# Kernel tuning notes

Hardware: AMD Instinct MI355X
Metric: run time of the kernel (lower is better)

## Reference

```python
import jax, jax.numpy as jnp
import numpy as np

N_NODES = 50000
N_EDGES = 1600000
IN_FEAT = 256
HID = IN_FEAT // 2  # 128
OUT_FEAT = 256


def setup_inputs() -> dict:
    key = jax.random.key(0)
    ks = jax.random.split(key, 10)
    x = jax.random.normal(ks[0], (N_NODES, IN_FEAT), dtype=jnp.float32)
    w = jax.random.uniform(ks[1], (N_EDGES, 1), dtype=jnp.float32)
    src = jax.random.randint(ks[2], (N_EDGES,), 0, N_NODES, dtype=jnp.int32)
    dst = jax.random.randint(ks[3], (N_EDGES,), 0, N_NODES, dtype=jnp.int32)
    s = 1.0 / np.sqrt(IN_FEAT)
    W_node = jax.random.uniform(ks[4], (IN_FEAT, HID), jnp.float32, -s, s)
    b_node = jax.random.uniform(ks[5], (HID,), jnp.float32, -s, s)
    W_edge = jax.random.uniform(ks[6], (IN_FEAT, HID), jnp.float32, -s, s)
    b_edge = jax.random.uniform(ks[7], (HID,), jnp.float32, -s, s)
    s2 = 1.0 / np.sqrt(HID)
    W_mlp = jax.random.uniform(ks[8], (HID, OUT_FEAT), jnp.float32, -s2, s2)
    b_mlp = jax.random.uniform(ks[9], (OUT_FEAT,), jnp.float32, -s2, s2)
    return {"x": x, "w": w, "src": src, "dst": dst,
            "W_node": W_node, "b_node": b_node,
            "W_edge": W_edge, "b_edge": b_edge,
            "W_mlp": W_mlp, "b_mlp": b_mlp}


def reference(x, w, src, dst, W_node, b_node, W_edge, b_edge, W_mlp, b_mlp):
    # message[v] = sum_{(u->v) in E} x[u] * w_e   (src_mul_edge + sum)
    message = jax.ops.segment_sum(x[src] * w, dst, num_segments=x.shape[0])  # [N, in_feat]
    h = (x @ W_node + b_node) + (message @ W_edge + b_edge)  # [N, in_feat//2]
    # NOTE: original uses nn.LeakyReLU(True) -> negative_slope=1.0 (identity);
    # replicated faithfully.
    h = jax.nn.leaky_relu(h, negative_slope=1.0)
    return h @ W_mlp + b_mlp  # [N, out_feat]
```

## Files before the change

kernel.cpp:

```cpp
#include <hip/hip_runtime.h>


constexpr int N_NODES  = 50000;
constexpr int N_EDGES  = 1600000;
constexpr int IN_FEAT  = 256;
constexpr int HID      = 128;
constexpr int OUT_FEAT = 256;

constexpr int BIN_SZ   = 32;
constexpr int N_BINS   = (N_NODES + BIN_SZ - 1) / BIN_SZ;
constexpr int CAPBIN   = 1536;
constexpr int EPB      = 4096;
constexpr int N_CBLK   = (N_EDGES + EPB - 1) / EPB;
constexpr int GRID_M   = (N_NODES + 127) / 128;
constexpr int N_G1BLK  = GRID_M * 2;

typedef __attribute__((ext_vector_type(8))) short bf16x8;
typedef __attribute__((ext_vector_type(8))) unsigned short u16x8;
typedef __attribute__((ext_vector_type(4))) float f32x4;

static __device__ __forceinline__ unsigned short f2bf(float f) {
    unsigned u = __builtin_bit_cast(unsigned, f);
    u += 0x7FFF + ((u >> 16) & 1);
    return (unsigned short)(u >> 16);
}
static __device__ __forceinline__ float bflo(unsigned u) {
    return __builtin_bit_cast(float, u << 16);
}
static __device__ __forceinline__ float bfhi(unsigned u) {
    return __builtin_bit_cast(float, u & 0xFFFF0000u);
}

__global__ __launch_bounds__(256) void k0_convert(
    const float* __restrict__ Wn, const float* __restrict__ We,
    const float* __restrict__ Wm,
    unsigned short* __restrict__ Wcat_t, unsigned short* __restrict__ Wmt)
{
    int n = blockIdx.x;
    int k = threadIdx.x;
    float v = (n < HID) ? Wn[(size_t)k * HID + n] : We[(size_t)k * HID + (n - HID)];
    Wcat_t[(size_t)n * IN_FEAT + k] = f2bf(v);
    if (k < HID) Wmt[(size_t)n * HID + k] = f2bf(Wm[(size_t)k * OUT_FEAT + n]);
}

union SharedU {
    struct {
        int  hist[N_BINS];
        int  gbase[N_BINS];
        int  wsum[8];
        int  stot;
        int2 sorted[EPB];
    } bc;
    struct {
        unsigned short As[128][64];
        unsigned short Bs[128][64];
    } g1;
};

__global__ __launch_bounds__(512, 4) void fuse1(
    const int* __restrict__ src, const int* __restrict__ dst,
    const float* __restrict__ w, int* __restrict__ cursor,
    int2* __restrict__ entries,
    const float* __restrict__ x, const unsigned short* __restrict__ Wcat_t,
    const float* __restrict__ bn, const float* __restrict__ be,
    float* __restrict__ h0, unsigned short* __restrict__ ybf)
{
    __shared__ SharedU sh;
    const int t = threadIdx.x;
    const int wave = t >> 6, lane = t & 63;

    if (blockIdx.x < N_CBLK) {
        const int e0 = blockIdx.x * EPB;

        for (int i = t; i < N_BINS; i += 512) sh.bc.hist[i] = 0;
        __syncthreads();

        int meta[8], wb[8], rk[8], bin[8];
        #pragma unroll
        for (int k = 0; k < 8; ++k) {
            int e = e0 + t + k * 512;
            bin[k] = -1;
            if (e < N_EDGES) {
                int d = dst[e];
                int b = d >> 5;
                bin[k]  = b;
                meta[k] = src[e] | ((d & 31) << 16) | (b << 21);
                wb[k]   = __float_as_int(w[e]);
                rk[k]   = atomicAdd(&sh.bc.hist[b], 1);
            }
        }
        __syncthreads();

        const int b4 = t * 4;
        int c0 = 0, c1 = 0, c2 = 0, c3 = 0;
        if (b4 + 0 < N_BINS) c0 = sh.bc.hist[b4 + 0];
        if (b4 + 1 < N_BINS) c1 = sh.bc.hist[b4 + 1];
        if (b4 + 2 < N_BINS) c2 = sh.bc.hist[b4 + 2];
        if (b4 + 3 < N_BINS) c3 = sh.bc.hist[b4 + 3];
        const int s = c0 + c1 + c2 + c3;
        int pre = s;
        #pragma unroll
        for (int off = 1; off < 64; off <<= 1) {
            int o = __shfl_up(pre, off, 64);
            if (lane >= off) pre += o;
        }
        if (lane == 63) sh.bc.wsum[wave] = pre;
        __syncthreads();
        if (t == 0) {
            int r = 0;
            #pragma unroll
            for (int q = 0; q < 8; ++q) { int v = sh.bc.wsum[q]; sh.bc.wsum[q] = r; r += v; }
            sh.bc.stot = r;
        }
        __syncthreads();
        const int tb = sh.bc.wsum[wave] + pre - s;

        if (b4 + 0 < N_BINS) {
            sh.bc.hist[b4 + 0]  = tb;
            sh.bc.gbase[b4 + 0] = c0 ? atomicAdd(&cursor[b4 + 0], c0) : 0;
        }
        if (b4 + 1 < N_BINS) {
            sh.bc.hist[b4 + 1]  = tb + c0;
            sh.bc.gbase[b4 + 1] = c1 ? atomicAdd(&cursor[b4 + 1], c1) : 0;
        }
        if (b4 + 2 < N_BINS) {
            sh.bc.hist[b4 + 2]  = tb + c0 + c1;
            sh.bc.gbase[b4 + 2] = c2 ? atomicAdd(&cursor[b4 + 2], c2) : 0;
        }
        if (b4 + 3 < N_BINS) {
            sh.bc.hist[b4 + 3]  = tb + c0 + c1 + c2;
            sh.bc.gbase[b4 + 3] = c3 ? atomicAdd(&cursor[b4 + 3], c3) : 0;
        }
        __syncthreads();

        #pragma unroll
        for (int k = 0; k < 8; ++k)
            if (bin[k] >= 0)
                sh.bc.sorted[sh.bc.hist[bin[k]] + rk[k]] = make_int2(meta[k], wb[k]);
        __syncthreads();

        const int tot = sh.bc.stot;
        #pragma unroll
        for (int k = 0; k < 8; ++k) {
            int i = t + k * 512;
            if (i < tot) {
                int2 q = sh.bc.sorted[i];
                int b = ((unsigned)q.x) >> 21;
                int r = i - sh.bc.hist[b];
                int g = sh.bc.gbase[b] + r;
                if (g < CAPBIN)
                    entries[(size_t)b * CAPBIN + g] = make_int2(q.x & 0x1FFFFF, q.y);
            }
        }
    } else {
        const int bid2 = blockIdx.x - N_CBLK;
        const int m0 = (bid2 >> 1) * 128;
        const int nhalf = bid2 & 1;
        const int n0r = nhalf * 128;

        const int wm = wave >> 2, wn = wave & 3;
        const int la = lane & 15, kq = lane >> 4;
        const int srow = t >> 3, sc8 = t & 7;

        f32x4 acc[4][2];
        const f32x4 zero = {0.f, 0.f, 0.f, 0.f};
        #pragma unroll
        for (int i = 0; i < 4; ++i)
            #pragma unroll
            for (int j = 0; j < 2; ++j) acc[i][j] = zero;

        const float4* xg = (const float4*)x;

        for (int kt = 0; kt < 4; ++kt) {
            if (kt) __syncthreads();
            #pragma unroll
            for (int i = 0; i < 2; ++i) {
                int row = srow + i * 64;
                int node = m0 + row;
                float4 v0 = make_float4(0.f, 0.f, 0.f, 0.f), v1 = v0;
                if (node < N_NODES) {
                    v0 = xg[(size_t)node * 64 + kt * 16 + sc8 * 2];
                    v1 = xg[(size_t)node * 64 + kt * 16 + sc8 * 2 + 1];
                }
                u16x8 b;
                b[0] = f2bf(v0.x); b[1] = f2bf(v0.y); b[2] = f2bf(v0.z); b[3] = f2bf(v0.w);
                b[4] = f2bf(v1.x); b[5] = f2bf(v1.y); b[6] = f2bf(v1.z); b[7] = f2bf(v1.w);
                *(u16x8*)&sh.g1.As[row][(sc8 ^ (row & 7)) * 8] = b;
            }
            #pragma unroll
            for (int i = 0; i < 2; ++i) {
                int row = srow + i * 64;
                float4 v = *(const float4*)(
                    Wcat_t + (size_t)(n0r + row) * IN_FEAT + kt * 64 + sc8 * 8);
                *(float4*)&sh.g1.Bs[row][(sc8 ^ (row & 7)) * 8] = v;
            }
            __syncthreads();

            #pragma unroll
            for (int ks = 0; ks < 2; ++ks) {
                bf16x8 a[4], b[2];
                #pragma unroll
                for (int i = 0; i < 4; ++i) {
                    int row = wm * 64 + i * 16 + la;
                    a[i] = *(const bf16x8*)&sh.g1.As[row][((ks * 4 + kq) ^ (row & 7)) * 8];
                }
                #pragma unroll
                for (int j = 0; j < 2; ++j) {
                    int row = wn * 32 + j * 16 + la;
                    b[j] = *(const bf16x8*)&sh.g1.Bs[row][((ks * 4 + kq) ^ (row & 7)) * 8];
                }
                #pragma unroll
                for (int i = 0; i < 4; ++i)
                    #pragma unroll
                    for (int j = 0; j < 2; ++j)
                        acc[i][j] = __builtin_amdgcn_mfma_f32_16x16x32_bf16(
                            a[i], b[j], acc[i][j], 0, 0, 0);
            }
        }

        float bias[2];
        if (nhalf == 0) {
            #pragma unroll
            for (int j = 0; j < 2; ++j) {
                int n = wn * 32 + j * 16 + la;
                bias[j] = bn[n] + be[n];
            }
        }
        #pragma unroll
        for (int i = 0; i < 4; ++i) {
            int mbase = m0 + wm * 64 + i * 16 + kq * 4;
            #pragma unroll
            for (int j = 0; j < 2; ++j) {
                int n = wn * 32 + j * 16 + la;
                #pragma unroll
                for (int r = 0; r < 4; ++r) {
                    int m = mbase + r;
                    if (m < N_NODES) {
                        if (nhalf == 0)
                            h0[(size_t)m * HID + n] = acc[i][j][r] + bias[j];
                        else
                            ybf[(size_t)m * HID + n] = f2bf(acc[i][j][r]);
                    }
                }
            }
        }
    }
}

__global__ __launch_bounds__(512, 4) void fuse2(
    const unsigned short* __restrict__ ybf, const float* __restrict__ h0,
    const int* __restrict__ cursor, const int2* __restrict__ entries,
    const unsigned short* __restrict__ Wmt, const float* __restrict__ bm,
    float* __restrict__ out)
{
    __shared__ unsigned short As[128][128];
    __shared__ int2 sorted[CAPBIN];
    __shared__ int  cnt32[BIN_SZ];
    __shared__ int  offs32[BIN_SZ];

    const int t = threadIdx.x;
    const int wave = t >> 6, lane = t & 63;
    const int m0 = blockIdx.x * 128;
    const int bin0 = blockIdx.x * 4;

    for (int sb = 0; sb < 4; ++sb) {
        const int bin = bin0 + sb;
        const int tot = (bin < N_BINS) ? min(cursor[bin], CAPBIN) : 0;
        if (t < BIN_SZ) cnt32[t] = 0;
        __syncthreads();

        int2 held[3];
        int  hrank[3], hdloc[3];
        #pragma unroll
        for (int k = 0; k < 3; ++k) {
            hdloc[k] = -1;
            int g = t + k * 512;
            if (g < tot) {
                int2 ep = entries[(size_t)bin * CAPBIN + g];
                int dloc = ep.x >> 16;
                held[k]  = make_int2(ep.x & 0xFFFF, ep.y);
                hdloc[k] = dloc;
                hrank[k] = atomicAdd(&cnt32[dloc], 1);
            }
        }
        __syncthreads();

        if (wave == 0) {
            int v = (lane < BIN_SZ) ? cnt32[lane] : 0;
            int sum = v;
            #pragma unroll
            for (int off = 1; off < BIN_SZ; off <<= 1) {
                int o = __shfl_up(sum, off, 64);
                if (lane >= off) sum += o;
            }
            if (lane < BIN_SZ) offs32[lane] = sum - v;
        }
        __syncthreads();

        #pragma unroll
        for (int k = 0; k < 3; ++k)
            if (hdloc[k] >= 0)
                sorted[offs32[hdloc[k]] + hrank[k]] = held[k];
        __syncthreads();

        #pragma unroll
        for (int n4 = 0; n4 < 4; ++n4) {
            const int nl = wave * 4 + n4;
            const int row = sb * 32 + nl;
            const int node = bin * BIN_SZ + nl;
            const int beg = offs32[nl];
            const int c = cnt32[nl];
            float a0 = 0.f, a1 = 0.f;
            int j = 0;
            for (; j + 8 <= c; j += 8) {
                int2 q[8]; unsigned u[8];
                #pragma unroll
                for (int e = 0; e < 8; ++e) q[e] = sorted[beg + j + e];
                #pragma unroll
                for (int e = 0; e < 8; ++e)
                    u[e] = *(const unsigned*)&ybf[(size_t)q[e].x * HID + 2 * lane];
                #pragma unroll
                for (int e = 0; e < 8; ++e) {
                    float wq = __int_as_float(q[e].y);
                    a0 += wq * bflo(u[e]); a1 += wq * bfhi(u[e]);
                }
            }
            for (; j < c; ++j) {
                int2 q = sorted[beg + j];
                unsigned u = *(const unsigned*)&ybf[(size_t)q.x * HID + 2 * lane];
                float wq = __int_as_float(q.y);
                a0 += wq * bflo(u); a1 += wq * bfhi(u);
            }
            float2 hv = make_float2(0.f, 0.f);
            if (node < N_NODES)
                hv = *(const float2*)&h0[(size_t)node * HID + 2 * lane];
            unsigned rp = ((unsigned)f2bf(hv.y + a1) << 16)
                        | (unsigned)f2bf(hv.x + a0);
            int g8 = (lane >> 2) ^ (row & 7);
            *(unsigned*)((char*)&As[row][0] + g8 * 16 + (lane & 3) * 4) = rp;
        }
        __syncthreads();
    }

    const int wm = wave >> 2, wn = wave & 3;
    const int la = lane & 15, kq = lane >> 4;

    f32x4 acc[4][4];
    const f32x4 zero = {0.f, 0.f, 0.f, 0.f};
    #pragma unroll
    for (int i = 0; i < 4; ++i)
        #pragma unroll
        for (int j = 0; j < 4; ++j) acc[i][j] = zero;

    #pragma unroll
    for (int ks = 0; ks < 4; ++ks) {
        bf16x8 a[4], b[4];
        #pragma unroll
        for (int i = 0; i < 4; ++i) {
            int row = wm * 64 + i * 16 + la;
            a[i] = *(const bf16x8*)&As[row][((ks * 4 + kq) ^ (row & 7)) * 8];
        }
        #pragma unroll
        for (int j = 0; j < 4; ++j) {
            int n = wn * 64 + j * 16 + la;
            b[j] = *(const bf16x8*)(Wmt + (size_t)n * HID + ks * 32 + kq * 8);
        }
        #pragma unroll
        for (int i = 0; i < 4; ++i)
            #pragma unroll
            for (int j = 0; j < 4; ++j)
                acc[i][j] = __builtin_amdgcn_mfma_f32_16x16x32_bf16(
                    a[i], b[j], acc[i][j], 0, 0, 0);
    }

    #pragma unroll
    for (int i = 0; i < 4; ++i) {
        int mbase = m0 + wm * 64 + i * 16 + kq * 4;
        #pragma unroll
        for (int j = 0; j < 4; ++j) {
            int n = wn * 64 + j * 16 + la;
            float bv = bm[n];
            #pragma unroll
            for (int r = 0; r < 4; ++r) {
                int m = mbase + r;
                if (m < N_NODES)
                    out[(size_t)m * OUT_FEAT + n] = acc[i][j][r] + bv;
            }
        }
    }
}

extern "C" void kernel_launch(void* const* d_in, const int* in_sizes, int n_in,
                              void* d_out, int out_size, void* d_ws, size_t ws_size,
                              hipStream_t stream) {
    const float* x   = (const float*)d_in[0];
    const float* w   = (const float*)d_in[1];
    const int*   src = (const int*)d_in[2];
    const int*   dst = (const int*)d_in[3];
    const float* Wn  = (const float*)d_in[4];
    const float* bn  = (const float*)d_in[5];
    const float* We  = (const float*)d_in[6];
    const float* be  = (const float*)d_in[7];
    const float* Wm  = (const float*)d_in[8];
    const float* bm  = (const float*)d_in[9];
    float* out = (float*)d_out;

    char* p = (char*)d_ws;
    float*          h0      = (float*)p;          p += (size_t)N_NODES * HID * 4;
    unsigned short* ybf     = (unsigned short*)p; p += (size_t)N_NODES * HID * 2;
    int2*           entries = (int2*)p;           p += (size_t)N_BINS * CAPBIN * 8;
    unsigned short* Wcat_t  = (unsigned short*)p; p += (size_t)256 * IN_FEAT * 2;
    unsigned short* Wmt     = (unsigned short*)p; p += (size_t)OUT_FEAT * HID * 2;
    int*            cursor  = (int*)p;            p += (size_t)N_BINS * 4;

    dim3 blk(256);

    hipMemsetAsync(cursor, 0, (size_t)N_BINS * 4, stream);
    k0_convert<<<256, blk, 0, stream>>>(Wn, We, Wm, Wcat_t, Wmt);
    fuse1<<<N_CBLK + N_G1BLK, dim3(512), 0, stream>>>(
        src, dst, w, cursor, entries, x, Wcat_t, bn, be, h0, ybf);
    fuse2<<<GRID_M, dim3(512), 0, stream>>>(ybf, h0, cursor, entries, Wmt, bm, out);
}
```

Baseline: 270.9 us.

## Launch one fuse2 block per 32-node bin instead of per 128 nodes

fuse2 now handles a single 32-node bin per block rather than looping over four bins serially, and the final MLP GEMM is cut to 32 rows per block. The grid grows from about 391 to about 1563 blocks, and shared memory per block shrinks. The goal is more parallelism and occupancy for the latency-bound gather and sort phase. In exchange, each block reloads the Wmt tile for only 32 rows, and the wm split now gives two waves duplicate-free 16-row slices of a small MFMA.

New measurement: 267.4 us. About the same (-1.3%).

```diff
diff --git a/kernel.cpp b/kernel.cpp
--- a/kernel.cpp
+++ b/kernel.cpp
@@ -253,139 +253,121 @@
     const unsigned short* __restrict__ Wmt, const float* __restrict__ bm,
     float* __restrict__ out)
 {
-    __shared__ unsigned short As[128][128];
     __shared__ int2 sorted[CAPBIN];
+    __shared__ unsigned short As[32][128];
     __shared__ int  cnt32[BIN_SZ];
     __shared__ int  offs32[BIN_SZ];
 
     const int t = threadIdx.x;
     const int wave = t >> 6, lane = t & 63;
-    const int m0 = blockIdx.x * 128;
-    const int bin0 = blockIdx.x * 4;
-
-    for (int sb = 0; sb < 4; ++sb) {
-        const int bin = bin0 + sb;
-        const int tot = (bin < N_BINS) ? min(cursor[bin], CAPBIN) : 0;
-        if (t < BIN_SZ) cnt32[t] = 0;
-        __syncthreads();
-
-        int2 held[3];
-        int  hrank[3], hdloc[3];
-        #pragma unroll
-        for (int k = 0; k < 3; ++k) {
-            hdloc[k] = -1;
-            int g = t + k * 512;
-            if (g < tot) {
-                int2 ep = entries[(size_t)bin * CAPBIN + g];
-                int dloc = ep.x >> 16;
-                held[k]  = make_int2(ep.x & 0xFFFF, ep.y);
-                hdloc[k] = dloc;
-                hrank[k] = atomicAdd(&cnt32[dloc], 1);
-            }
-        }
-        __syncthreads();
-
-        if (wave == 0) {
-            int v = (lane < BIN_SZ) ? cnt32[lane] : 0;
-            int sum = v;
-            #pragma unroll
-            for (int off = 1; off < BIN_SZ; off <<= 1) {
-                int o = __shfl_up(sum, off, 64);
-                if (lane >= off) sum += o;
-            }
-            if (lane < BIN_SZ) offs32[lane] = sum - v;
-        }
-        __syncthreads();
-
-        #pragma unroll
-        for (int k = 0; k < 3; ++k)
-            if (hdloc[k] >= 0)
-                sorted[offs32[hdloc[k]] + hrank[k]] = held[k];
-        __syncthreads();
-
-        #pragma unroll
-        for (int n4 = 0; n4 < 4; ++n4) {
-            const int nl = wave * 4 + n4;
-            const int row = sb * 32 + nl;
-            const int node = bin * BIN_SZ + nl;
-            const int beg = offs32[nl];
-            const int c = cnt32[nl];
-            float a0 = 0.f, a1 = 0.f;
-            int j = 0;
-            for (; j + 8 <= c; j += 8) {
-                int2 q[8]; unsigned u[8];
-                #pragma unroll
-                for (int e = 0; e < 8; ++e) q[e] = sorted[beg + j + e];
-                #pragma unroll
-                for (int e = 0; e < 8; ++e)
-                    u[e] = *(const unsigned*)&ybf[(size_t)q[e].x * HID + 2 * lane];
-                #pragma unroll
-                for (int e = 0; e < 8; ++e) {
-                    float wq = __int_as_float(q[e].y);
-                    a0 += wq * bflo(u[e]); a1 += wq * bfhi(u[e]);
-                }
-            }
-            for (; j < c; ++j) {
-                int2 q = sorted[beg + j];
-                unsigned u = *(const unsigned*)&ybf[(size_t)q.x * HID + 2 * lane];
-                float wq = __int_as_float(q.y);
-                a0 += wq * bflo(u); a1 += wq * bfhi(u);
-            }
-            float2 hv = make_float2(0.f, 0.f);
-            if (node < N_NODES)
-                hv = *(const float2*)&h0[(size_t)node * HID + 2 * lane];
-            unsigned rp = ((unsigned)f2bf(hv.y + a1) << 16)
-                        | (unsigned)f2bf(hv.x + a0);
-            int g8 = (lane >> 2) ^ (row & 7);
-            *(unsigned*)((char*)&As[row][0] + g8 * 16 + (lane & 3) * 4) = rp;
-        }
-        __syncthreads();
-    }
+    const int bin = blockIdx.x;
+    const int node0 = bin * BIN_SZ;
+
+    const int tot = min(cursor[bin], CAPBIN);
+    if (t < BIN_SZ) cnt32[t] = 0;
+    __syncthreads();
+
+    int2 held[3];
+    int  hrank[3], hdloc[3];
+    #pragma unroll
+    for (int k = 0; k < 3; ++k) {
+        hdloc[k] = -1;
+        int g = t + k * 512;
+        if (g < tot) {
+            int2 ep = entries[(size_t)bin * CAPBIN + g];
+            int dloc = ep.x >> 16;
+            held[k]  = make_int2(ep.x & 0xFFFF, ep.y);
+            hdloc[k] = dloc;
+            hrank[k] = atomicAdd(&cnt32[dloc], 1);
+        }
+    }
+    __syncthreads();
+
+    if (wave == 0) {
+        int v = (lane < BIN_SZ) ? cnt32[lane] : 0;
+        int sum = v;
+        #pragma unroll
+        for (int off = 1; off < BIN_SZ; off <<= 1) {
+            int o = __shfl_up(sum, off, 64);
+            if (lane >= off) sum += o;
+        }
+        if (lane < BIN_SZ) offs32[lane] = sum - v;
+    }
+    __syncthreads();
+
+    #pragma unroll
+    for (int k = 0; k < 3; ++k)
+        if (hdloc[k] >= 0)
+            sorted[offs32[hdloc[k]] + hrank[k]] = held[k];
+    __syncthreads();
+
+    #pragma unroll
+    for (int n4 = 0; n4 < 4; ++n4) {
+        const int nl = wave * 4 + n4;
+        const int node = node0 + nl;
+        const int beg = offs32[nl];
+        const int c = cnt32[nl];
+        float a0 = 0.f, a1 = 0.f;
+        int j = 0;
+        for (; j + 8 <= c; j += 8) {
+            int2 q[8]; unsigned u[8];
+            #pragma unroll
+            for (int e = 0; e < 8; ++e) q[e] = sorted[beg + j + e];
+            #pragma unroll
+            for (int e = 0; e < 8; ++e)
+                u[e] = *(const unsigned*)&ybf[(size_t)q[e].x * HID + 2 * lane];
+            #pragma unroll
+            for (int e = 0; e < 8; ++e) {
+                float wq = __int_as_float(q[e].y);
+                a0 += wq * bflo(u[e]); a1 += wq * bfhi(u[e]);
+            }
+        }
+        for (; j < c; ++j) {
+            int2 q = sorted[beg + j];
+            unsigned u = *(const unsigned*)&ybf[(size_t)q.x * HID + 2 * lane];
+            float wq = __int_as_float(q.y);
+            a0 += wq * bflo(u); a1 += wq * bfhi(u);
+        }
+        float2 hv = make_float2(0.f, 0.f);
+        if (node < N_NODES)
+            hv = *(const float2*)&h0[(size_t)node * HID + 2 * lane];
+        unsigned rp = ((unsigned)f2bf(hv.y + a1) << 16)
+                    | (unsigned)f2bf(hv.x + a0);
+        int g8 = (lane >> 2) ^ (nl & 7);
+        *(unsigned*)((char*)&As[nl][0] + g8 * 16 + (lane & 3) * 4) = rp;
+    }
+    __syncthreads();
 
     const int wm = wave >> 2, wn = wave & 3;
     const int la = lane & 15, kq = lane >> 4;
 
-    f32x4 acc[4][4];
+    f32x4 acc[4];
     const f32x4 zero = {0.f, 0.f, 0.f, 0.f};
     #pragma unroll
-    for (int i = 0; i < 4; ++i)
-        #pragma unroll
-        for (int j = 0; j < 4; ++j) acc[i][j] = zero;
+    for (int j = 0; j < 4; ++j) acc[j] = zero;
 
     #pragma unroll
     for (int ks = 0; ks < 4; ++ks) {
-        bf16x8 a[4], b[4];
-        #pragma unroll
-        for (int i = 0; i < 4; ++i) {
-            int row = wm * 64 + i * 16 + la;
-            a[i] = *(const bf16x8*)&As[row][((ks * 4 + kq) ^ (row & 7)) * 8];
-        }
+        int row = wm * 16 + la;
+        bf16x8 a = *(const bf16x8*)&As[row][(((ks * 4 + kq) ^ (row & 7))) * 8];
         #pragma unroll
         for (int j = 0; j < 4; ++j) {
             int n = wn * 64 + j * 16 + la;
-            b[j] = *(const bf16x8*)(Wmt + (size_t)n * HID + ks * 32 + kq * 8);
-        }
-        #pragma unroll
-        for (int i = 0; i < 4; ++i)
-            #pragma unroll
-            for (int j = 0; j < 4; ++j)
-                acc[i][j] = __builtin_amdgcn_mfma_f32_16x16x32_bf16(
-                    a[i], b[j], acc[i][j], 0, 0, 0);
-    }
-
-    #pragma unroll
-    for (int i = 0; i < 4; ++i) {
-        int mbase = m0 + wm * 64 + i * 16 + kq * 4;
-        #pragma unroll
-        for (int j = 0; j < 4; ++j) {
-            int n = wn * 64 + j * 16 + la;
-            float bv = bm[n];
-            #pragma unroll
-            for (int r = 0; r < 4; ++r) {
-                int m = mbase + r;
-                if (m < N_NODES)
-                    out[(size_t)m * OUT_FEAT + n] = acc[i][j][r] + bv;
-            }
+            bf16x8 b = *(const bf16x8*)(Wmt + (size_t)n * HID + ks * 32 + kq * 8);
+            acc[j] = __builtin_amdgcn_mfma_f32_16x16x32_bf16(a, b, acc[j], 0, 0, 0);
+        }
+    }
+
+    const int mbase = node0 + wm * 16 + kq * 4;
+    #pragma unroll
+    for (int j = 0; j < 4; ++j) {
+        int n = wn * 64 + j * 16 + la;
+        float bv = bm[n];
+        #pragma unroll
+        for (int r = 0; r < 4; ++r) {
+            int m = mbase + r;
+            if (m < N_NODES)
+                out[(size_t)m * OUT_FEAT + n] = acc[j][r] + bv;
         }
     }
 }
@@ -419,5 +401,5 @@
     k0_convert<<<256, blk, 0, stream>>>(Wn, We, Wm, Wcat_t, Wmt);
     fuse1<<<N_CBLK + N_G1BLK, dim3(512), 0, stream>>>(
         src, dst, w, cursor, entries, x, Wcat_t, bn, be, h0, ybf);
-    fuse2<<<GRID_M, dim3(512), 0, stream>>>(ybf, h0, cursor, entries, Wmt, bm, out);
-}
+    fuse2<<<N_BINS, dim3(512), 0, stream>>>(ybf, h0, cursor, entries, Wmt, bm, out);
+}
```
